# Optimization experiments

Hardware: AMD Instinct MI355X
Metric: run time of the kernel (lower is better)

The kernel has to match this reference:

```python
import jax, jax.numpy as jnp
import numpy as np

NUM_HEADS = 4
NUM_GROUPS = 32
EPS = 1e-5

def setup_inputs() -> dict:
    key = jax.random.key(0)
    ks = jax.random.split(key, 3)
    B, C, H, W = 16, 512, 32, 32
    x = jax.random.normal(ks[0], (B, C, H, W), dtype=jnp.float32)
    gn_w = jnp.ones((C,), jnp.float32)
    gn_b = jnp.zeros((C,), jnp.float32)
    qkv_w = jax.random.normal(ks[1], (3 * C, C), dtype=jnp.float32) * (C ** -0.5)
    qkv_b = jnp.zeros((3 * C,), jnp.float32)
    proj_w = jax.random.normal(ks[2], (C, C), dtype=jnp.float32) * (C ** -0.5)
    proj_b = jnp.zeros((C,), jnp.float32)
    return {"x": x, "gn_w": gn_w, "gn_b": gn_b, "qkv_w": qkv_w,
            "qkv_b": qkv_b, "proj_w": proj_w, "proj_b": proj_b}

def group_norm(x, w, b):
    B, C, H, W = x.shape
    xg = x.reshape(B, NUM_GROUPS, C // NUM_GROUPS, H, W)
    mean = xg.mean(axis=(2, 3, 4), keepdims=True)
    var = xg.var(axis=(2, 3, 4), keepdims=True)
    xg = (xg - mean) * jax.lax.rsqrt(var + EPS)
    x = xg.reshape(B, C, H, W)
    return x * w[None, :, None, None] + b[None, :, None, None]

def reference(x, gn_w, gn_b, qkv_w, qkv_b, proj_w, proj_b):
    B, C, H, W = x.shape
    hd = C // NUM_HEADS
    h = group_norm(x, gn_w, gn_b)
    # 1x1 conv == channel matmul
    qkv = jnp.einsum('oc,bchw->bohw', qkv_w, h) + qkv_b[None, :, None, None]
    q, k, v = jnp.split(qkv, 3, axis=1)
    N = H * W
    q = q.reshape(B, NUM_HEADS, hd, N)
    k = k.reshape(B, NUM_HEADS, hd, N)
    v = v.reshape(B, NUM_HEADS, hd, N)
    scale = hd ** -0.5
    attn = jnp.einsum('bhcn,bhcm->bhnm', q, k) * scale
    attn = jax.nn.softmax(attn, axis=-1)
    o = jnp.einsum('bhnm,bhcm->bhcn', attn, v).reshape(B, C, H, W)
    o = jnp.einsum('oc,bchw->bohw', proj_w, o) + proj_b[None, :, None, None]
    return x + o
```

## Files before the change

### kernel.cpp

```cpp
#include <hip/hip_runtime.h>

typedef __attribute__((ext_vector_type(4))) float f32x4;
typedef __attribute__((ext_vector_type(8))) short s16x8;

#define MFMA16(a, b, c) __builtin_amdgcn_mfma_f32_16x16x32_bf16((a), (b), (c), 0, 0, 0)

__device__ __forceinline__ unsigned short f2bf(float f) {
    union { float f; unsigned u; } v; v.f = f;
    unsigned u = v.u + 0x7FFFu + ((v.u >> 16) & 1u);
    return (unsigned short)(u >> 16);
}

__device__ __forceinline__ unsigned cvtpk(float lo, float hi) {
    unsigned r;
    asm("v_cvt_pk_bf16_f32 %0, %1, %2" : "=v"(r) : "v"(lo), "v"(hi));
    return r;
}

__device__ __forceinline__ float exp2f_fast(float x) {
    float r;
    asm("v_exp_f32 %0, %1" : "=v"(r) : "v"(x));
    return r;
}

__device__ __forceinline__ void gll16(const unsigned short* g, unsigned short* l) {
    __builtin_amdgcn_global_load_lds((const __attribute__((address_space(1))) void*)g,
                                     (__attribute__((address_space(3))) void*)l, 16, 0, 0);
}

__global__ __launch_bounds__(256) void k_wconv(const float* __restrict__ qkv_w,
                                               const float* __restrict__ proj_w,
                                               unsigned short* __restrict__ wout) {
    int i = blockIdx.x * 256 + threadIdx.x;
    const int NQ = 3 * 512 * 512;
    float v = (i < NQ) ? qkv_w[i] : proj_w[i - NQ];
    wout[i] = f2bf(v);
}

__global__ __launch_bounds__(256) void k_gn(const float* __restrict__ x,
                                            const float* __restrict__ gnw,
                                            const float* __restrict__ gnb,
                                            unsigned short* __restrict__ h_t) {
    int bg = blockIdx.x;
    int b = bg >> 5, g = bg & 31;
    int t = threadIdx.x;
    const float4* p = (const float4*)(x + (size_t)bg * 16384);
    float s = 0.f, ss = 0.f;
    for (int i = t; i < 4096; i += 256) {
        float4 v = p[i];
        s += v.x + v.y + v.z + v.w;
        ss += v.x * v.x + v.y * v.y + v.z * v.z + v.w * v.w;
    }
    for (int w = 1; w < 64; w <<= 1) { s += __shfl_xor(s, w); ss += __shfl_xor(ss, w); }
    __shared__ float rs[4], rss[4], mv[2];
    __shared__ unsigned short ldt[1024][18];
    int wid = t >> 6;
    if ((t & 63) == 0) { rs[wid] = s; rss[wid] = ss; }
    __syncthreads();
    if (t == 0) {
        float S = rs[0] + rs[1] + rs[2] + rs[3];
        float SS = rss[0] + rss[1] + rss[2] + rss[3];
        float mean = S * (1.f / 16384.f);
        float var = SS * (1.f / 16384.f) - mean * mean;
        mv[0] = mean; mv[1] = rsqrtf(var + 1e-5f);
    }
    __syncthreads();
    int c = t >> 4, f4 = t & 15;
    float mean = mv[0], rstd = mv[1];
    float sc = gnw[g * 16 + c] * rstd;
    float sh = gnb[g * 16 + c] - mean * sc;
    const float4* pc = (const float4*)(x + ((size_t)(b * 512 + g * 16 + c)) * 1024);
#pragma unroll
    for (int i = 0; i < 16; ++i) {
        int n = i * 64 + f4 * 4;
        float4 v = pc[n >> 2];
        ldt[n + 0][c] = f2bf(v.x * sc + sh);
        ldt[n + 1][c] = f2bf(v.y * sc + sh);
        ldt[n + 2][c] = f2bf(v.z * sc + sh);
        ldt[n + 3][c] = f2bf(v.w * sc + sh);
    }
    __syncthreads();
    int half = t & 1;
#pragma unroll
    for (int i = 0; i < 8; ++i) {
        int row = i * 128 + (t >> 1);
        *(uint4*)(h_t + ((size_t)(b * 1024 + row)) * 512 + g * 16 + half * 8) =
            *(const uint4*)(&ldt[row][half * 8]);
    }
}

template<int MODE>
__global__ __launch_bounds__(512, 6) void k_gemm(const unsigned short* __restrict__ A,
                                                 const unsigned short* __restrict__ Bt,
                                                 const float* __restrict__ bias,
                                                 unsigned short* __restrict__ Qo,
                                                 unsigned short* __restrict__ Ko,
                                                 unsigned short* __restrict__ Vo,
                                                 const float* __restrict__ xres,
                                                 float* __restrict__ out) {
    const int Kd = 512;
    int id = blockIdx.x;
    int xcd = id & 7, j = id >> 3;
    int nt = xcd + 8 * (j & 15);
    int mt = j >> 4;
    int t = threadIdx.x, wid = t >> 6, lane = t & 63;
    int lm = lane & 15, q4 = lane >> 4;
    int wm = wid >> 2, wn = wid & 3;
    __shared__ unsigned short ldsA[2][4096];
    __shared__ unsigned short ldsB[2][4096];
    int m0 = mt * 128, n0 = nt * 128;

    int r = t >> 2;
    int cc = (t & 3) ^ (r & 3);
    const unsigned short* gA = A + (size_t)(m0 + r) * Kd + cc * 8;
    const unsigned short* gB = Bt + (size_t)(n0 + r) * Kd + cc * 8;
    unsigned short* dA[2] = { &ldsA[0][wid * 512], &ldsA[1][wid * 512] };
    unsigned short* dB[2] = { &ldsB[0][wid * 512], &ldsB[1][wid * 512] };

    f32x4 z = {0.f, 0.f, 0.f, 0.f};
    f32x4 acc[4][2];
#pragma unroll
    for (int fi = 0; fi < 4; ++fi)
#pragma unroll
        for (int fj = 0; fj < 2; ++fj) acc[fi][fj] = z;

    gll16(gA, dA[0]); gll16(gB, dB[0]);
    gA += 32; gB += 32;

    const int NK = 16;
    for (int ks = 0; ks < NK; ++ks) {
        int cur = ks & 1;
        if (ks + 1 < NK) {
            gll16(gA, dA[cur ^ 1]); gll16(gB, dB[cur ^ 1]);
            gA += 32; gB += 32;
            asm volatile("s_waitcnt vmcnt(2)" ::: "memory");
        } else {
            asm volatile("s_waitcnt vmcnt(0)" ::: "memory");
        }
        __builtin_amdgcn_s_barrier();
        asm volatile("" ::: "memory");
        const unsigned short* lA = ldsA[cur];
        const unsigned short* lB = ldsB[cur];
        s16x8 af[4], bg[2];
#pragma unroll
        for (int fi = 0; fi < 4; ++fi) {
            int rA = wm * 64 + fi * 16 + lm;
            af[fi] = *(const s16x8*)&lA[(rA * 4 + (q4 ^ (lm & 3))) * 8];
        }
#pragma unroll
        for (int fj = 0; fj < 2; ++fj) {
            int rB = wn * 32 + fj * 16 + lm;
            bg[fj] = *(const s16x8*)&lB[(rB * 4 + (q4 ^ (lm & 3))) * 8];
        }
        if (MODE == 0) {
#pragma unroll
            for (int fi = 0; fi < 4; ++fi)
#pragma unroll
                for (int fj = 0; fj < 2; ++fj) acc[fi][fj] = MFMA16(af[fi], bg[fj], acc[fi][fj]);
        } else {
#pragma unroll
            for (int fi = 0; fi < 4; ++fi)
#pragma unroll
                for (int fj = 0; fj < 2; ++fj) acc[fi][fj] = MFMA16(bg[fj], af[fi], acc[fi][fj]);
        }
        asm volatile("" ::: "memory");
        __builtin_amdgcn_s_barrier();
    }

    int b = nt >> 3;
    if (MODE == 0) {
        int part = mt >> 2;
        int head = mt & 3;
        int bh = b * 4 + head;
        const float qscale = 0.08838834764831845f * 1.4426950408889634f;
#pragma unroll
        for (int fi = 0; fi < 4; ++fi) {
            int ddb = wm * 64 + fi * 16 + 4 * q4;
            float bv[4];
#pragma unroll
            for (int i = 0; i < 4; ++i) bv[i] = bias[mt * 128 + ddb + i];
#pragma unroll
            for (int fj = 0; fj < 2; ++fj) {
                int n = ((nt & 7) << 7) + wn * 32 + fj * 16 + lm;
                f32x4 v = acc[fi][fj];
                uint2 pr;
                if (part == 0) {
                    pr.x = cvtpk((v[0] + bv[0]) * qscale, (v[1] + bv[1]) * qscale);
                    pr.y = cvtpk((v[2] + bv[2]) * qscale, (v[3] + bv[3]) * qscale);
                    *(uint2*)(Qo + ((size_t)bh * 1024 + n) * 128 + ddb) = pr;
                } else {
                    pr.x = cvtpk(v[0] + bv[0], v[1] + bv[1]);
                    pr.y = cvtpk(v[2] + bv[2], v[3] + bv[3]);
                    *(uint2*)(Ko + ((size_t)bh * 1024 + n) * 128 + ddb) = pr;
                }
            }
        }
    } else if (MODE == 1) {
        int bh = b * 4 + mt;
#pragma unroll
        for (int fi = 0; fi < 4; ++fi) {
            int d = wm * 64 + fi * 16 + lm;
            float bv = bias[mt * 128 + d];
#pragma unroll
            for (int fj = 0; fj < 2; ++fj) {
                int np = ((nt & 7) << 7) + wn * 32 + q4 * 8 + fj * 4;
                f32x4 v = acc[fi][fj];
                uint2 pr;
                pr.x = cvtpk(v[0] + bv, v[1] + bv);
                pr.y = cvtpk(v[2] + bv, v[3] + bv);
                *(uint2*)(Vo + ((size_t)bh * 128 + d) * 1024 + np) = pr;
            }
        }
    } else {
#pragma unroll
        for (int fi = 0; fi < 4; ++fi) {
            int oc = m0 + wm * 64 + fi * 16 + lm;
            float bv = bias[oc];
#pragma unroll
            for (int fj = 0; fj < 2; ++fj) {
                int n = ((nt & 7) << 7) + wn * 32 + fj * 16 + 4 * q4;
                size_t idx = ((size_t)b * 512 + oc) * 1024 + n;
                float4 xr = *(const float4*)&xres[idx];
                f32x4 v = acc[fi][fj];
                float4 o;
                o.x = xr.x + bv + v[0];
                o.y = xr.y + bv + v[1];
                o.z = xr.z + bv + v[2];
                o.w = xr.w + bv + v[3];
                *(float4*)&out[idx] = o;
            }
        }
    }
}

__global__ __launch_bounds__(128, 2) void k_attn(const unsigned short* __restrict__ Q,
                                                 const unsigned short* __restrict__ K,
                                                 const unsigned short* __restrict__ V,
                                                 unsigned short* __restrict__ o_t) {
    int id = blockIdx.y * 8 + blockIdx.x;
    int bh = (id & 7) + ((id >> 7) << 3);
    int qb = (id >> 3) & 15;
    int t = threadIdx.x, wid = t >> 6, lane = t & 63;
    int lm = lane & 15, q4 = lane >> 4;
    __shared__ unsigned short ldsK[2][4096];
    __shared__ unsigned short ldsV[2][4096];
    const unsigned short* Qg = Q + ((size_t)bh * 1024 + qb * 64 + wid * 32) * 128;
    const unsigned short* Kg = K + (size_t)bh * 1024 * 128;
    const unsigned short* Vg = V + (size_t)bh * 128 * 1024;

    s16x8 qf0[4], qf1[4];
#pragma unroll
    for (int dc = 0; dc < 4; ++dc) {
        qf0[dc] = *(const s16x8*)&Qg[lm * 128 + dc * 32 + q4 * 8];
        qf1[dc] = *(const s16x8*)&Qg[(16 + lm) * 128 + dc * 32 + q4 * 8];
    }

    const unsigned short* gk[4];
    const unsigned short* gv[4];
    unsigned short* lkd[2][4];
    unsigned short* lvd[2][4];
#pragma unroll
    for (int h = 0; h < 4; ++h) {
        int cib = h * 128 + wid * 64;
        int ci = cib + lane;
        int mr = ci >> 4, cl = ci & 15;
        gk[h] = Kg + mr * 128 + (cl ^ (mr & 7)) * 8;
        int d = ci >> 2, kc = ci & 3;
        gv[h] = Vg + (size_t)d * 1024 + (kc ^ ((d >> 1) & 3)) * 8;
        lkd[0][h] = &ldsK[0][cib * 8];
        lkd[1][h] = &ldsK[1][cib * 8];
        lvd[0][h] = &ldsV[0][cib * 8];
        lvd[1][h] = &ldsV[1][cib * 8];
    }
#pragma unroll
    for (int h = 0; h < 4; ++h) { gll16(gk[h], lkd[0][h]); gll16(gv[h], lvd[0][h]); }
#pragma unroll
    for (int h = 0; h < 4; ++h) { gk[h] += 4096; gv[h] += 32; }

    f32x4 z = {0.f, 0.f, 0.f, 0.f};
    f32x4 oa[8], ob[8];
#pragma unroll
    for (int i = 0; i < 8; ++i) { oa[i] = z; ob[i] = z; }
    f32x4 lca = z, lcb = z;
    float mra = 0.f, mrb = 0.f;
    union { s16x8 v; unsigned u[4]; } ones;
    ones.u[0] = ones.u[1] = ones.u[2] = ones.u[3] = 0x3F803F80u;

    for (int ms = 0; ms < 32; ++ms) {
        int cur = ms & 1;
        if (ms < 31) {
            int nb = cur ^ 1;
#pragma unroll
            for (int h = 0; h < 4; ++h) { gll16(gk[h], lkd[nb][h]); gll16(gv[h], lvd[nb][h]); }
#pragma unroll
            for (int h = 0; h < 4; ++h) { gk[h] += 4096; gv[h] += 32; }
            asm volatile("s_waitcnt vmcnt(8)" ::: "memory");
        } else {
            asm volatile("s_waitcnt vmcnt(0)" ::: "memory");
        }
        __builtin_amdgcn_s_barrier();
        const unsigned short* lK = ldsK[cur];
        const unsigned short* lV = ldsV[cur];

        float nia = -mra, nib = -mrb;
        f32x4 sa = {nia, nia, nia, nia}, sb = {nib, nib, nib, nib};
        f32x4 sc = sa, sd = sb;
        __builtin_amdgcn_s_setprio(1);
#pragma unroll
        for (int dc = 0; dc < 4; ++dc) {
            int sw = ((dc * 4 + q4) ^ (lm & 7)) * 8;
            s16x8 k0 = *(const s16x8*)&lK[lm * 128 + sw];
            s16x8 k1 = *(const s16x8*)&lK[(16 + lm) * 128 + sw];
            sa = MFMA16(k0, qf0[dc], sa);
            sb = MFMA16(k0, qf1[dc], sb);
            sc = MFMA16(k1, qf0[dc], sc);
            sd = MFMA16(k1, qf1[dc], sd);
        }
        __builtin_amdgcn_s_setprio(0);

        float tma = fmaxf(fmaxf(fmaxf(sa[0], sa[1]), fmaxf(sa[2], sa[3])),
                          fmaxf(fmaxf(sc[0], sc[1]), fmaxf(sc[2], sc[3])));
        float tmb = fmaxf(fmaxf(fmaxf(sb[0], sb[1]), fmaxf(sb[2], sb[3])),
                          fmaxf(fmaxf(sd[0], sd[1]), fmaxf(sd[2], sd[3])));
        if (!__all(tma <= 8.f && tmb <= 8.f)) {
            tma = fmaxf(tma, __shfl_xor(tma, 16));
            tma = fmaxf(tma, __shfl_xor(tma, 32));
            tmb = fmaxf(tmb, __shfl_xor(tmb, 16));
            tmb = fmaxf(tmb, __shfl_xor(tmb, 32));
            float da_ = fmaxf(tma, 0.f), db_ = fmaxf(tmb, 0.f);
            float ca = exp2f_fast(-da_), cb = exp2f_fast(-db_);
            mra += da_; mrb += db_;
#pragma unroll
            for (int i = 0; i < 4; ++i) {
                sa[i] -= da_; sc[i] -= da_;
                sb[i] -= db_; sd[i] -= db_;
            }
            lca[0] *= ca; lcb[0] *= cb;
#pragma unroll
            for (int t8 = 0; t8 < 8; ++t8)
#pragma unroll
                for (int i = 0; i < 4; ++i) { oa[t8][i] *= ca; ob[t8][i] *= cb; }
        }
        float pa[8], pb[8];
#pragma unroll
        for (int i = 0; i < 4; ++i) {
            pa[i]     = exp2f_fast(sa[i]);
            pa[4 + i] = exp2f_fast(sc[i]);
            pb[i]     = exp2f_fast(sb[i]);
            pb[4 + i] = exp2f_fast(sd[i]);
        }
        union { s16x8 v; unsigned u[4]; } fa, fb;
        fa.u[0] = cvtpk(pa[0], pa[1]); fa.u[1] = cvtpk(pa[2], pa[3]);
        fa.u[2] = cvtpk(pa[4], pa[5]); fa.u[3] = cvtpk(pa[6], pa[7]);
        fb.u[0] = cvtpk(pb[0], pb[1]); fb.u[1] = cvtpk(pb[2], pb[3]);
        fb.u[2] = cvtpk(pb[4], pb[5]); fb.u[3] = cvtpk(pb[6], pb[7]);
        lca = MFMA16(ones.v, fa.v, lca);
        lcb = MFMA16(ones.v, fb.v, lcb);

        __builtin_amdgcn_s_setprio(1);
#pragma unroll
        for (int t8 = 0; t8 < 8; ++t8) {
            int r = t8 * 16 + lm;
            s16x8 vf = *(const s16x8*)&lV[r * 32 + ((q4 ^ ((lm >> 1) & 3)) * 8)];
            oa[t8] = MFMA16(vf, fa.v, oa[t8]);
            ob[t8] = MFMA16(vf, fb.v, ob[t8]);
        }
        __builtin_amdgcn_s_setprio(0);
        __builtin_amdgcn_s_barrier();
    }

    float inva = 1.f / lca[0], invb = 1.f / lcb[0];
    int b = bh >> 2, head = bh & 3;
    size_t rowa = (size_t)b * 1024 + qb * 64 + wid * 32 + lm;
    unsigned short* da = o_t + rowa * 512 + head * 128;
    unsigned short* db = da + (size_t)16 * 512;
#pragma unroll
    for (int t8 = 0; t8 < 8; ++t8) {
        uint2 pr;
        pr.x = cvtpk(oa[t8][0] * inva, oa[t8][1] * inva);
        pr.y = cvtpk(oa[t8][2] * inva, oa[t8][3] * inva);
        *(uint2*)&da[t8 * 16 + q4 * 4] = pr;
        pr.x = cvtpk(ob[t8][0] * invb, ob[t8][1] * invb);
        pr.y = cvtpk(ob[t8][2] * invb, ob[t8][3] * invb);
        *(uint2*)&db[t8 * 16 + q4 * 4] = pr;
    }
}

extern "C" void kernel_launch(void* const* d_in, const int* in_sizes, int n_in,
                              void* d_out, int out_size, void* d_ws, size_t ws_size,
                              hipStream_t stream) {
    const float* x = (const float*)d_in[0];
    const float* gnw = (const float*)d_in[1];
    const float* gnb = (const float*)d_in[2];
    const float* qkvw = (const float*)d_in[3];
    const float* qkvb = (const float*)d_in[4];
    const float* projw = (const float*)d_in[5];
    const float* projb = (const float*)d_in[6];
    float* out = (float*)d_out;
    char* ws = (char*)d_ws;

    unsigned short* wq = (unsigned short*)(ws);
    unsigned short* wp = (unsigned short*)(ws + 1572864);
    unsigned short* ht = (unsigned short*)(ws + 2101248);
    unsigned short* Qb = (unsigned short*)(ws + 18878464);
    unsigned short* Kb = (unsigned short*)(ws + 35655680);
    unsigned short* Vb = (unsigned short*)(ws + 52432896);
    unsigned short* ot = ht;

    k_wconv<<<dim3(4096), dim3(256), 0, stream>>>(qkvw, projw, wq);
    k_gn<<<dim3(512), dim3(256), 0, stream>>>(x, gnw, gnb, ht);
    k_gemm<0><<<dim3(1024), dim3(512), 0, stream>>>(wq, ht, qkvb, Qb, Kb, nullptr, nullptr, nullptr);
    k_gemm<1><<<dim3(512), dim3(512), 0, stream>>>(wq + 8 * 128 * 512, ht, qkvb + 1024,
                                                   nullptr, nullptr, Vb, nullptr, nullptr);
    k_attn<<<dim3(8, 128), dim3(128), 0, stream>>>(Qb, Kb, Vb, ot);
    k_gemm<2><<<dim3(512), dim3(512), 0, stream>>>(wp, ot, projb, nullptr, nullptr, nullptr, x, out);
}
```

Before: 134.3 us.

## Load K/V fragments straight from global into registers in single-wave attention blocks

The attention kernel drops its LDS double-buffered K/V staging and the block barriers. Each 64-thread block now handles 32 queries and prefetches the next K and V MFMA fragments from global memory directly into registers, overlapping those loads with the current step's compute. The softmax switches to a conventional running-max form, and the row sum is accumulated in registers with a final shuffle reduction instead of a ones-matrix MFMA. This removes LDS traffic and synchronisation, but each wave now fetches K/V separately, which doubles global/L2 reads and raises register pressure.

```diff
diff --git a/kernel.cpp b/kernel.cpp
--- a/kernel.cpp
+++ b/kernel.cpp
@@ -233,20 +233,19 @@
     }
 }
 
-__global__ __launch_bounds__(128, 2) void k_attn(const unsigned short* __restrict__ Q,
-                                                 const unsigned short* __restrict__ K,
-                                                 const unsigned short* __restrict__ V,
-                                                 unsigned short* __restrict__ o_t) {
-    int id = blockIdx.y * 8 + blockIdx.x;
-    int bh = (id & 7) + ((id >> 7) << 3);
-    int qb = (id >> 3) & 15;
-    int t = threadIdx.x, wid = t >> 6, lane = t & 63;
+__global__ __launch_bounds__(64, 2) void k_attn(const unsigned short* __restrict__ Q,
+                                                const unsigned short* __restrict__ K,
+                                                const unsigned short* __restrict__ V,
+                                                unsigned short* __restrict__ o_t) {
+    int id = blockIdx.x;
+    int xcd = id & 7, j = id >> 3;
+    int qb = j & 31;
+    int bh = xcd + 8 * (j >> 5);
+    int lane = threadIdx.x & 63;
     int lm = lane & 15, q4 = lane >> 4;
-    __shared__ unsigned short ldsK[2][4096];
-    __shared__ unsigned short ldsV[2][4096];
-    const unsigned short* Qg = Q + ((size_t)bh * 1024 + qb * 64 + wid * 32) * 128;
-    const unsigned short* Kg = K + (size_t)bh * 1024 * 128;
-    const unsigned short* Vg = V + (size_t)bh * 128 * 1024;
+    const unsigned short* Qg = Q + ((size_t)bh * 1024 + qb * 32) * 128;
+    const unsigned short* Kbase = K + (size_t)bh * 1024 * 128 + lm * 128 + q4 * 8;
+    const unsigned short* Vbase = V + (size_t)bh * 128 * 1024 + lm * 1024 + q4 * 8;
 
     s16x8 qf0[4], qf1[4];
 #pragma unroll
@@ -255,66 +254,36 @@
         qf1[dc] = *(const s16x8*)&Qg[(16 + lm) * 128 + dc * 32 + q4 * 8];
     }
 
-    const unsigned short* gk[4];
-    const unsigned short* gv[4];
-    unsigned short* lkd[2][4];
-    unsigned short* lvd[2][4];
-#pragma unroll
-    for (int h = 0; h < 4; ++h) {
-        int cib = h * 128 + wid * 64;
-        int ci = cib + lane;
-        int mr = ci >> 4, cl = ci & 15;
-        gk[h] = Kg + mr * 128 + (cl ^ (mr & 7)) * 8;
-        int d = ci >> 2, kc = ci & 3;
-        gv[h] = Vg + (size_t)d * 1024 + (kc ^ ((d >> 1) & 3)) * 8;
-        lkd[0][h] = &ldsK[0][cib * 8];
-        lkd[1][h] = &ldsK[1][cib * 8];
-        lvd[0][h] = &ldsV[0][cib * 8];
-        lvd[1][h] = &ldsV[1][cib * 8];
-    }
-#pragma unroll
-    for (int h = 0; h < 4; ++h) { gll16(gk[h], lkd[0][h]); gll16(gv[h], lvd[0][h]); }
-#pragma unroll
-    for (int h = 0; h < 4; ++h) { gk[h] += 4096; gv[h] += 32; }
-
     f32x4 z = {0.f, 0.f, 0.f, 0.f};
     f32x4 oa[8], ob[8];
 #pragma unroll
     for (int i = 0; i < 8; ++i) { oa[i] = z; ob[i] = z; }
-    f32x4 lca = z, lcb = z;
-    float mra = 0.f, mrb = 0.f;
-    union { s16x8 v; unsigned u[4]; } ones;
-    ones.u[0] = ones.u[1] = ones.u[2] = ones.u[3] = 0x3F803F80u;
-
-    for (int ms = 0; ms < 32; ++ms) {
-        int cur = ms & 1;
-        if (ms < 31) {
-            int nb = cur ^ 1;
-#pragma unroll
-            for (int h = 0; h < 4; ++h) { gll16(gk[h], lkd[nb][h]); gll16(gv[h], lvd[nb][h]); }
-#pragma unroll
-            for (int h = 0; h < 4; ++h) { gk[h] += 4096; gv[h] += 32; }
-            asm volatile("s_waitcnt vmcnt(8)" ::: "memory");
-        } else {
-            asm volatile("s_waitcnt vmcnt(0)" ::: "memory");
-        }
-        __builtin_amdgcn_s_barrier();
-        const unsigned short* lK = ldsK[cur];
-        const unsigned short* lV = ldsV[cur];
-
-        float nia = -mra, nib = -mrb;
-        f32x4 sa = {nia, nia, nia, nia}, sb = {nib, nib, nib, nib};
-        f32x4 sc = sa, sd = sb;
+    float mra = -1e30f, mrb = -1e30f, lpa = 0.f, lpb = 0.f;
+
+    s16x8 kA[8], kB[8], vv[8];
+#pragma unroll
+    for (int dc = 0; dc < 4; ++dc) {
+        kA[dc]     = *(const s16x8*)(Kbase + dc * 32);
+        kA[4 + dc] = *(const s16x8*)(Kbase + 2048 + dc * 32);
+    }
+#pragma unroll
+    for (int t8 = 0; t8 < 8; ++t8)
+        vv[t8] = *(const s16x8*)(Vbase + t8 * 16384);
+
+    auto step = [&](s16x8 (&cur)[8], s16x8 (&nxt)[8], int m0n) {
+#pragma unroll
+        for (int dc = 0; dc < 4; ++dc) {
+            nxt[dc]     = *(const s16x8*)(Kbase + m0n * 128 + dc * 32);
+            nxt[4 + dc] = *(const s16x8*)(Kbase + m0n * 128 + 2048 + dc * 32);
+        }
+        f32x4 sa = z, sb = z, sc = z, sd = z;
         __builtin_amdgcn_s_setprio(1);
 #pragma unroll
         for (int dc = 0; dc < 4; ++dc) {
-            int sw = ((dc * 4 + q4) ^ (lm & 7)) * 8;
-            s16x8 k0 = *(const s16x8*)&lK[lm * 128 + sw];
-            s16x8 k1 = *(const s16x8*)&lK[(16 + lm) * 128 + sw];
-            sa = MFMA16(k0, qf0[dc], sa);
-            sb = MFMA16(k0, qf1[dc], sb);
-            sc = MFMA16(k1, qf0[dc], sc);
-            sd = MFMA16(k1, qf1[dc], sd);
+            sa = MFMA16(cur[dc], qf0[dc], sa);
+            sb = MFMA16(cur[dc], qf1[dc], sb);
+            sc = MFMA16(cur[4 + dc], qf0[dc], sc);
+            sd = MFMA16(cur[4 + dc], qf1[dc], sd);
         }
         __builtin_amdgcn_s_setprio(0);
 
@@ -322,56 +291,61 @@
                           fmaxf(fmaxf(sc[0], sc[1]), fmaxf(sc[2], sc[3])));
         float tmb = fmaxf(fmaxf(fmaxf(sb[0], sb[1]), fmaxf(sb[2], sb[3])),
                           fmaxf(fmaxf(sd[0], sd[1]), fmaxf(sd[2], sd[3])));
-        if (!__all(tma <= 8.f && tmb <= 8.f)) {
+        if (!__all(tma <= mra + 8.f && tmb <= mrb + 8.f)) {
             tma = fmaxf(tma, __shfl_xor(tma, 16));
             tma = fmaxf(tma, __shfl_xor(tma, 32));
             tmb = fmaxf(tmb, __shfl_xor(tmb, 16));
             tmb = fmaxf(tmb, __shfl_xor(tmb, 32));
-            float da_ = fmaxf(tma, 0.f), db_ = fmaxf(tmb, 0.f);
-            float ca = exp2f_fast(-da_), cb = exp2f_fast(-db_);
-            mra += da_; mrb += db_;
-#pragma unroll
-            for (int i = 0; i < 4; ++i) {
-                sa[i] -= da_; sc[i] -= da_;
-                sb[i] -= db_; sd[i] -= db_;
-            }
-            lca[0] *= ca; lcb[0] *= cb;
+            float mna = fmaxf(mra, tma), mnb = fmaxf(mrb, tmb);
+            float ca = exp2f_fast(mra - mna), cb = exp2f_fast(mrb - mnb);
+            lpa *= ca; lpb *= cb;
 #pragma unroll
             for (int t8 = 0; t8 < 8; ++t8)
 #pragma unroll
                 for (int i = 0; i < 4; ++i) { oa[t8][i] *= ca; ob[t8][i] *= cb; }
+            mra = mna; mrb = mnb;
         }
         float pa[8], pb[8];
 #pragma unroll
         for (int i = 0; i < 4; ++i) {
-            pa[i]     = exp2f_fast(sa[i]);
-            pa[4 + i] = exp2f_fast(sc[i]);
-            pb[i]     = exp2f_fast(sb[i]);
-            pb[4 + i] = exp2f_fast(sd[i]);
-        }
+            pa[i]     = exp2f_fast(sa[i] - mra);
+            pa[4 + i] = exp2f_fast(sc[i] - mra);
+            pb[i]     = exp2f_fast(sb[i] - mrb);
+            pb[4 + i] = exp2f_fast(sd[i] - mrb);
+        }
+#pragma unroll
+        for (int i = 0; i < 8; ++i) { lpa += pa[i]; lpb += pb[i]; }
         union { s16x8 v; unsigned u[4]; } fa, fb;
         fa.u[0] = cvtpk(pa[0], pa[1]); fa.u[1] = cvtpk(pa[2], pa[3]);
         fa.u[2] = cvtpk(pa[4], pa[5]); fa.u[3] = cvtpk(pa[6], pa[7]);
         fb.u[0] = cvtpk(pb[0], pb[1]); fb.u[1] = cvtpk(pb[2], pb[3]);
         fb.u[2] = cvtpk(pb[4], pb[5]); fb.u[3] = cvtpk(pb[6], pb[7]);
-        lca = MFMA16(ones.v, fa.v, lca);
-        lcb = MFMA16(ones.v, fb.v, lcb);
 
         __builtin_amdgcn_s_setprio(1);
 #pragma unroll
         for (int t8 = 0; t8 < 8; ++t8) {
-            int r = t8 * 16 + lm;
-            s16x8 vf = *(const s16x8*)&lV[r * 32 + ((q4 ^ ((lm >> 1) & 3)) * 8)];
-            oa[t8] = MFMA16(vf, fa.v, oa[t8]);
-            ob[t8] = MFMA16(vf, fb.v, ob[t8]);
+            oa[t8] = MFMA16(vv[t8], fa.v, oa[t8]);
+            ob[t8] = MFMA16(vv[t8], fb.v, ob[t8]);
         }
         __builtin_amdgcn_s_setprio(0);
-        __builtin_amdgcn_s_barrier();
-    }
-
-    float inva = 1.f / lca[0], invb = 1.f / lcb[0];
+#pragma unroll
+        for (int t8 = 0; t8 < 8; ++t8)
+            vv[t8] = *(const s16x8*)(Vbase + t8 * 16384 + m0n);
+    };
+
+#pragma unroll 1
+    for (int tt = 0; tt < 16; ++tt) {
+        int m1 = (2 * tt + 1) * 32;
+        int m2 = ((2 * tt + 2) & 31) * 32;
+        step(kA, kB, m1);
+        step(kB, kA, m2);
+    }
+
+    lpa += __shfl_xor(lpa, 16); lpa += __shfl_xor(lpa, 32);
+    lpb += __shfl_xor(lpb, 16); lpb += __shfl_xor(lpb, 32);
+    float inva = 1.f / lpa, invb = 1.f / lpb;
     int b = bh >> 2, head = bh & 3;
-    size_t rowa = (size_t)b * 1024 + qb * 64 + wid * 32 + lm;
+    size_t rowa = (size_t)b * 1024 + qb * 32 + lm;
     unsigned short* da = o_t + rowa * 512 + head * 128;
     unsigned short* db = da + (size_t)16 * 512;
 #pragma unroll
@@ -412,6 +386,6 @@
     k_gemm<0><<<dim3(1024), dim3(512), 0, stream>>>(wq, ht, qkvb, Qb, Kb, nullptr, nullptr, nullptr);
     k_gemm<1><<<dim3(512), dim3(512), 0, stream>>>(wq + 8 * 128 * 512, ht, qkvb + 1024,
                                                    nullptr, nullptr, Vb, nullptr, nullptr);
-    k_attn<<<dim3(8, 128), dim3(128), 0, stream>>>(Qb, Kb, Vb, ot);
+    k_attn<<<dim3(2048), dim3(64), 0, stream>>>(Qb, Kb, Vb, ot);
     k_gemm<2><<<dim3(512), dim3(512), 0, stream>>>(wp, ot, projb, nullptr, nullptr, nullptr, x, out);
 }
```

After: 206.5 us. 1.54x slower.
